# Kernel tuning notes

Hardware: AMD Instinct MI355X
Metric: run time of the kernel (lower is better)

Reference implementation:

```python
import jax, jax.numpy as jnp
import numpy as np

N_NODES = 100000
N_EDGES = 1600000
D_FEAT = 32
D_HID = 64
D_OUT = 64


def setup_inputs() -> dict:
    key = jax.random.key(0)
    ks = jax.random.split(key, 7)
    x = jax.random.normal(ks[0], (N_NODES, D_FEAT), dtype=jnp.float32)
    pos = jax.random.uniform(ks[1], (N_NODES, 3), dtype=jnp.float32) * 100.0
    # Fixed-size stand-in for radius_graph(pos, 5) output: (2, E) [source; target]
    edge_index = jax.random.randint(ks[2], (2, N_EDGES), 0, N_NODES, dtype=jnp.int64)
    d_in = D_FEAT + 3  # concat(x_j, pos_j - pos_i)
    W1 = jax.random.normal(ks[3], (d_in, D_HID), dtype=jnp.float32) / np.sqrt(d_in)
    b1 = jnp.zeros((D_HID,), dtype=jnp.float32)
    W2 = jax.random.normal(ks[4], (D_HID, D_OUT), dtype=jnp.float32) / np.sqrt(D_HID)
    b2 = jnp.zeros((D_OUT,), dtype=jnp.float32)
    return {"x": x, "pos": pos, "edge_index": edge_index,
            "W1": W1, "b1": b1, "W2": W2, "b2": b2}


def reference(x, pos, edge_index, W1, b1, W2, b2):
    n = x.shape[0]
    # PointNetConv default add_self_loops=True (radius_graph used loop=False)
    loops = jnp.arange(n, dtype=edge_index.dtype)
    src = jnp.concatenate([edge_index[0], loops])  # source j
    dst = jnp.concatenate([edge_index[1], loops])  # target i
    # gather: per-edge message input [E+N, d_feat+3]
    msg_in = jnp.concatenate([x[src], pos[src] - pos[dst]], axis=-1)
    # local_nn MLP
    h = jax.nn.relu(msg_in @ W1 + b1) @ W2 + b2
    # scatter: max-aggregate onto target nodes (PointConv aggr='max')
    out = jax.ops.segment_max(h, dst, num_segments=n)
    return out
```

## Files before the change

### kernel.cpp

```cpp
#include <hip/hip_runtime.h>
#include <math.h>

#define N_NODES 100000
#define N_EDGES 1600000
#define D_FEAT 32
#define D_HID 64
#define D_OUT 64
#define CAP 48
#define NPB 32
#define NBKT 3125
#define B1 256
#define E_PER_B1 6250
#define NB_NODE 1024

typedef _Float16 half8 __attribute__((ext_vector_type(8)));
typedef float f32x4  __attribute__((ext_vector_type(4)));

__device__ inline unsigned pk_subrelu(unsigned v, unsigned nq) {
    unsigned r;
    asm("v_pk_add_f16 %0, %1, %2\n\t"
        "v_pk_max_f16 %0, %0, 0"
        : "=v"(r) : "v"(v), "v"(nq));
    return r;
}

__global__ __launch_bounds__(256)
void node_kernel(const float* __restrict__ x,
                 const float* __restrict__ pos,
                 const float* __restrict__ W1,
                 const float* __restrict__ b1,
                 unsigned short* __restrict__ vb,
                 unsigned short* __restrict__ qb) {
    const int lane = threadIdx.x & 63;
    const int wid  = (blockIdx.x * blockDim.x + threadIdx.x) >> 6;
    const int nw   = (NB_NODE * 256) >> 6;

    float w[D_FEAT + 3];
#pragma unroll
    for (int f = 0; f < D_FEAT + 3; ++f)
        w[f] = W1[f * D_HID + lane];
    const float bb = b1[lane];

    for (int node = wid; node < N_NODES; node += nw) {
        const float* xr = x + (size_t)node * D_FEAT;
        float acc = bb;
#pragma unroll
        for (int f = 0; f < D_FEAT; ++f)
            acc = fmaf(xr[f], w[f], acc);

        const float* pr = pos + (size_t)node * 3;
        float qa = 0.0f;
#pragma unroll
        for (int p = 0; p < 3; ++p)
            qa = fmaf(pr[p], w[D_FEAT + p], qa);

        vb[(size_t)node * D_HID + lane] =
            __builtin_bit_cast(unsigned short, (_Float16)(acc + qa));
        qb[(size_t)node * D_HID + lane] =
            __builtin_bit_cast(unsigned short, (_Float16)(-qa));
    }
}

__global__ __launch_bounds__(1024)
void sort_kernel(const int* __restrict__ src,
                 const int* __restrict__ dst,
                 unsigned int* __restrict__ coarse,
                 int* __restrict__ dirT) {
    __shared__ int hist[NBKT];
    __shared__ int stage[E_PER_B1];
    __shared__ int wsum[16];

    const int tid  = threadIdx.x;
    const int lane = tid & 63;
    const int wv   = tid >> 6;
    const int e0   = blockIdx.x * E_PER_B1;

    for (int b = tid; b < NBKT; b += 1024) hist[b] = 0;
    __syncthreads();

    for (int e = e0 + tid; e < e0 + E_PER_B1; e += 1024)
        atomicAdd(&hist[dst[e] >> 5], 1);
    __syncthreads();

    const int i0 = tid * 4;
    int c[4];
    int sum = 0;
#pragma unroll
    for (int k = 0; k < 4; ++k) {
        c[k] = (i0 + k < NBKT) ? hist[i0 + k] : 0;
        sum += c[k];
    }
    int inc = sum;
#pragma unroll
    for (int d = 1; d < 64; d <<= 1) {
        int u = __shfl_up(inc, d, 64);
        if (lane >= d) inc += u;
    }
    if (lane == 63) wsum[wv] = inc;
    __syncthreads();
    if (wv == 0) {
        int s = (lane < 16) ? wsum[lane] : 0;
#pragma unroll
        for (int d = 1; d < 16; d <<= 1) {
            int u = __shfl_up(s, d, 64);
            if (lane >= d) s += u;
        }
        if (lane < 16) wsum[lane] = s;
    }
    __syncthreads();
    int excl = inc - sum + ((wv > 0) ? wsum[wv - 1] : 0);
#pragma unroll
    for (int k = 0; k < 4; ++k) {
        if (i0 + k < NBKT) hist[i0 + k] = excl;
        excl += c[k];
    }
    __syncthreads();

    for (int b = tid; b < NBKT; b += 1024)
        dirT[(size_t)b * B1 + blockIdx.x] = e0 + hist[b];
    __syncthreads();

    for (int e = e0 + tid; e < e0 + E_PER_B1; e += 1024) {
        int d = dst[e], s = src[e];
        int p = atomicAdd(&hist[d >> 5], 1);
        stage[p] = (int)(((unsigned)s << 5) | (unsigned)(d & 31));
    }
    __syncthreads();

    for (int i = tid; i < E_PER_B1; i += 1024)
        coarse[e0 + i] = (unsigned)stage[i];
}

__global__ __launch_bounds__(256)
void agg_kernel(const unsigned short* __restrict__ vb,
                const unsigned short* __restrict__ qb,
                const float* __restrict__ W2,
                const float* __restrict__ b2,
                const int* __restrict__ dirT,
                const unsigned int* __restrict__ coarse,
                float* __restrict__ out) {
    __shared__ int lcnt[NPB];
    __shared__ int lslots[NPB][CAP];

    const int tid  = threadIdx.x;
    const int lane = tid & 63;
    const int wave = tid >> 6;
    const int quad = lane >> 4;
    const int mrow = lane & 15;
    const int bkt  = blockIdx.x;
    const int nbase = bkt << 5;

    half8 bfrag[4][2];
#pragma unroll
    for (int t = 0; t < 4; ++t)
#pragma unroll
        for (int kh = 0; kh < 2; ++kh) {
            half8 f;
#pragma unroll
            for (int j = 0; j < 8; ++j)
                f[j] = (_Float16)W2[(kh * 32 + quad * 8 + j) * D_OUT + t * 16 + mrow];
            bfrag[t][kh] = f;
        }
    float bias[4];
#pragma unroll
    for (int t = 0; t < 4; ++t) bias[t] = b2[t * 16 + mrow];

    for (int i = tid; i < NPB; i += 256) lcnt[i] = 0;
    __syncthreads();
    {
        const int s0 = dirT[(size_t)bkt * B1 + tid];
        const int s1 = (bkt + 1 < NBKT) ? dirT[(size_t)(bkt + 1) * B1 + tid]
                                        : (tid + 1) * E_PER_B1;
        for (int j = s0; j < s1; ++j) {
            unsigned enc = coarse[j];
            int local = (int)(enc & 31u);
            int s     = (int)(enc >> 5);
            int p = atomicAdd(&lcnt[local], 1);
            if (p < CAP) lslots[local][p] = s;
        }
    }
    __syncthreads();

    for (int ln = wave; ln < NPB; ln += 4) {
        const int node = nbase + ln;

        const uint4 nq0 = *(const uint4*)(qb + (size_t)node * D_HID + quad * 8);
        const uint4 nq1 = *(const uint4*)(qb + (size_t)node * D_HID + 32 + quad * 8);

        int deg = lcnt[ln];
        if (deg > CAP) deg = CAP;
        const int rows = deg + 1;
        const int nbat = (rows + 15) >> 4;

        float rmax[4][4];
#pragma unroll
        for (int t = 0; t < 4; ++t)
#pragma unroll
            for (int r = 0; r < 4; ++r) rmax[t][r] = -INFINITY;

        for (int b = 0; b < nbat; ++b) {
            int idx = b * 16 + mrow;
            int idxc = (idx < CAP) ? idx : (CAP - 1);
            int s = (idx < deg) ? lslots[ln][idxc] : node;

            const uint4 v0 = *(const uint4*)(vb + (size_t)s * D_HID + quad * 8);
            const uint4 v1 = *(const uint4*)(vb + (size_t)s * D_HID + 32 + quad * 8);

            uint4 a0u, a1u;
            a0u.x = pk_subrelu(v0.x, nq0.x);
            a0u.y = pk_subrelu(v0.y, nq0.y);
            a0u.z = pk_subrelu(v0.z, nq0.z);
            a0u.w = pk_subrelu(v0.w, nq0.w);
            a1u.x = pk_subrelu(v1.x, nq1.x);
            a1u.y = pk_subrelu(v1.y, nq1.y);
            a1u.z = pk_subrelu(v1.z, nq1.z);
            a1u.w = pk_subrelu(v1.w, nq1.w);
            half8 a0 = __builtin_bit_cast(half8, a0u);
            half8 a1 = __builtin_bit_cast(half8, a1u);

#pragma unroll
            for (int t = 0; t < 4; ++t) {
                f32x4 acc = (f32x4){0.f, 0.f, 0.f, 0.f};
                acc = __builtin_amdgcn_mfma_f32_16x16x32_f16(a0, bfrag[t][0], acc, 0, 0, 0);
                acc = __builtin_amdgcn_mfma_f32_16x16x32_f16(a1, bfrag[t][1], acc, 0, 0, 0);
#pragma unroll
                for (int r = 0; r < 4; ++r)
                    rmax[t][r] = fmaxf(rmax[t][r], acc[r]);
            }
        }

        float fin[4];
#pragma unroll
        for (int t = 0; t < 4; ++t) {
            float m = fmaxf(fmaxf(rmax[t][0], rmax[t][1]), fmaxf(rmax[t][2], rmax[t][3]));
            m = fmaxf(m, __shfl_xor(m, 16, 64));
            m = fmaxf(m, __shfl_xor(m, 32, 64));
            fin[t] = m + bias[t];
        }
        float r = (quad == 0) ? fin[0] : (quad == 1) ? fin[1] : (quad == 2) ? fin[2] : fin[3];
        out[(size_t)node * D_OUT + lane] = r;
    }
}

extern "C" void kernel_launch(void* const* d_in, const int* in_sizes, int n_in,
                              void* d_out, int out_size, void* d_ws, size_t ws_size,
                              hipStream_t stream) {
    const float* x   = (const float*)d_in[0];
    const float* pos = (const float*)d_in[1];
    const int*   ei  = (const int*)d_in[2];
    const float* W1  = (const float*)d_in[3];
    const float* b1  = (const float*)d_in[4];
    const float* W2  = (const float*)d_in[5];
    const float* b2  = (const float*)d_in[6];
    float* out = (float*)d_out;

    char* ws = (char*)d_ws;
    unsigned short* vb   = (unsigned short*)ws;
    unsigned short* qb   = (unsigned short*)(ws + 12800000);
    unsigned int* coarse = (unsigned int*)(ws + 25600000);
    int*            dirT = (int*)(ws + 32000000);

    const int* src = ei;
    const int* dst = ei + N_EDGES;

    hipLaunchKernelGGL(sort_kernel, dim3(B1), dim3(1024), 0, stream,
                       src, dst, coarse, dirT);
    hipLaunchKernelGGL(node_kernel, dim3(NB_NODE), dim3(256), 0, stream,
                       x, pos, W1, b1, vb, qb);
    hipLaunchKernelGGL(agg_kernel, dim3(NBKT), dim3(256), 0, stream,
                       vb, qb, W2, b2, dirT, coarse, out);
}
```

Measured before the change: 199.6 us.

## Make aggregation kernel persistent with atomic work queue and pre-transposed fp16 W2

Turns the aggregation kernel into a persistent grid of 2048 blocks that claim 32-node buckets from a global atomic counter, so the per-block W2 fragment setup is paid once per block rather than once per bucket. W2 is also converted to fp16 and transposed once inside the sort kernel, so each block loads its MFMA B-fragments as vector loads instead of strided scalar float loads. This adds a memset, a global atomic and extra barriers per bucket, and with fewer resident blocks there may be less latency hiding for the gather loads.

```diff
diff --git a/kernel.cpp b/kernel.cpp
--- a/kernel.cpp
+++ b/kernel.cpp
@@ -12,6 +12,7 @@
 #define B1 256
 #define E_PER_B1 6250
 #define NB_NODE 1024
+#define AGG_B 2048
 
 typedef _Float16 half8 __attribute__((ext_vector_type(8)));
 typedef float f32x4  __attribute__((ext_vector_type(4)));
@@ -65,7 +66,9 @@
 void sort_kernel(const int* __restrict__ src,
                  const int* __restrict__ dst,
                  unsigned int* __restrict__ coarse,
-                 int* __restrict__ dirT) {
+                 int* __restrict__ dirT,
+                 const float* __restrict__ W2,
+                 unsigned short* __restrict__ W2T) {
     __shared__ int hist[NBKT];
     __shared__ int stage[E_PER_B1];
     __shared__ int wsum[16];
@@ -75,6 +78,14 @@
     const int wv   = tid >> 6;
     const int e0   = blockIdx.x * E_PER_B1;
 
+    if (blockIdx.x == 0) {
+        for (int i = tid; i < D_HID * D_OUT; i += 1024) {
+            float w = W2[i];
+            W2T[(size_t)(i & 63) * D_HID + (i >> 6)] =
+                __builtin_bit_cast(unsigned short, (_Float16)w);
+        }
+    }
+
     for (int b = tid; b < NBKT; b += 1024) hist[b] = 0;
     __syncthreads();
 
@@ -134,111 +145,117 @@
 __global__ __launch_bounds__(256)
 void agg_kernel(const unsigned short* __restrict__ vb,
                 const unsigned short* __restrict__ qb,
-                const float* __restrict__ W2,
+                const unsigned short* __restrict__ W2T,
                 const float* __restrict__ b2,
                 const int* __restrict__ dirT,
                 const unsigned int* __restrict__ coarse,
+                int* __restrict__ ctr,
                 float* __restrict__ out) {
     __shared__ int lcnt[NPB];
     __shared__ int lslots[NPB][CAP];
+    __shared__ int sbkt;
 
     const int tid  = threadIdx.x;
     const int lane = tid & 63;
     const int wave = tid >> 6;
     const int quad = lane >> 4;
     const int mrow = lane & 15;
-    const int bkt  = blockIdx.x;
-    const int nbase = bkt << 5;
 
     half8 bfrag[4][2];
 #pragma unroll
     for (int t = 0; t < 4; ++t)
 #pragma unroll
-        for (int kh = 0; kh < 2; ++kh) {
-            half8 f;
-#pragma unroll
-            for (int j = 0; j < 8; ++j)
-                f[j] = (_Float16)W2[(kh * 32 + quad * 8 + j) * D_OUT + t * 16 + mrow];
-            bfrag[t][kh] = f;
-        }
+        for (int kh = 0; kh < 2; ++kh)
+            bfrag[t][kh] = *(const half8*)(W2T + (size_t)(t * 16 + mrow) * D_HID
+                                               + kh * 32 + quad * 8);
     float bias[4];
 #pragma unroll
     for (int t = 0; t < 4; ++t) bias[t] = b2[t * 16 + mrow];
 
-    for (int i = tid; i < NPB; i += 256) lcnt[i] = 0;
-    __syncthreads();
-    {
-        const int s0 = dirT[(size_t)bkt * B1 + tid];
-        const int s1 = (bkt + 1 < NBKT) ? dirT[(size_t)(bkt + 1) * B1 + tid]
-                                        : (tid + 1) * E_PER_B1;
-        for (int j = s0; j < s1; ++j) {
-            unsigned enc = coarse[j];
-            int local = (int)(enc & 31u);
-            int s     = (int)(enc >> 5);
-            int p = atomicAdd(&lcnt[local], 1);
-            if (p < CAP) lslots[local][p] = s;
-        }
-    }
-    __syncthreads();
-
-    for (int ln = wave; ln < NPB; ln += 4) {
-        const int node = nbase + ln;
-
-        const uint4 nq0 = *(const uint4*)(qb + (size_t)node * D_HID + quad * 8);
-        const uint4 nq1 = *(const uint4*)(qb + (size_t)node * D_HID + 32 + quad * 8);
-
-        int deg = lcnt[ln];
-        if (deg > CAP) deg = CAP;
-        const int rows = deg + 1;
-        const int nbat = (rows + 15) >> 4;
-
-        float rmax[4][4];
-#pragma unroll
-        for (int t = 0; t < 4; ++t)
-#pragma unroll
-            for (int r = 0; r < 4; ++r) rmax[t][r] = -INFINITY;
-
-        for (int b = 0; b < nbat; ++b) {
-            int idx = b * 16 + mrow;
-            int idxc = (idx < CAP) ? idx : (CAP - 1);
-            int s = (idx < deg) ? lslots[ln][idxc] : node;
-
-            const uint4 v0 = *(const uint4*)(vb + (size_t)s * D_HID + quad * 8);
-            const uint4 v1 = *(const uint4*)(vb + (size_t)s * D_HID + 32 + quad * 8);
-
-            uint4 a0u, a1u;
-            a0u.x = pk_subrelu(v0.x, nq0.x);
-            a0u.y = pk_subrelu(v0.y, nq0.y);
-            a0u.z = pk_subrelu(v0.z, nq0.z);
-            a0u.w = pk_subrelu(v0.w, nq0.w);
-            a1u.x = pk_subrelu(v1.x, nq1.x);
-            a1u.y = pk_subrelu(v1.y, nq1.y);
-            a1u.z = pk_subrelu(v1.z, nq1.z);
-            a1u.w = pk_subrelu(v1.w, nq1.w);
-            half8 a0 = __builtin_bit_cast(half8, a0u);
-            half8 a1 = __builtin_bit_cast(half8, a1u);
-
+    while (true) {
+        if (tid == 0) sbkt = atomicAdd(ctr, 1);
+        __syncthreads();
+        const int bkt = sbkt;
+        if (bkt >= NBKT) break;
+        const int nbase = bkt << 5;
+
+        for (int i = tid; i < NPB; i += 256) lcnt[i] = 0;
+        __syncthreads();
+
+        {
+            const int s0 = dirT[(size_t)bkt * B1 + tid];
+            const int s1 = (bkt + 1 < NBKT) ? dirT[(size_t)(bkt + 1) * B1 + tid]
+                                            : (tid + 1) * E_PER_B1;
+            for (int j = s0; j < s1; ++j) {
+                unsigned enc = coarse[j];
+                int local = (int)(enc & 31u);
+                int s     = (int)(enc >> 5);
+                int p = atomicAdd(&lcnt[local], 1);
+                if (p < CAP) lslots[local][p] = s;
+            }
+        }
+        __syncthreads();
+
+        for (int ln = wave; ln < NPB; ln += 4) {
+            const int node = nbase + ln;
+
+            const uint4 nq0 = *(const uint4*)(qb + (size_t)node * D_HID + quad * 8);
+            const uint4 nq1 = *(const uint4*)(qb + (size_t)node * D_HID + 32 + quad * 8);
+
+            int deg = lcnt[ln];
+            if (deg > CAP) deg = CAP;
+            const int rows = deg + 1;
+            const int nbat = (rows + 15) >> 4;
+
+            float rmax[4][4];
+#pragma unroll
+            for (int t = 0; t < 4; ++t)
+#pragma unroll
+                for (int r = 0; r < 4; ++r) rmax[t][r] = -INFINITY;
+
+            for (int b = 0; b < nbat; ++b) {
+                int idx = b * 16 + mrow;
+                int idxc = (idx < CAP) ? idx : (CAP - 1);
+                int s = (idx < deg) ? lslots[ln][idxc] : node;
+
+                const uint4 v0 = *(const uint4*)(vb + (size_t)s * D_HID + quad * 8);
+                const uint4 v1 = *(const uint4*)(vb + (size_t)s * D_HID + 32 + quad * 8);
+
+                uint4 a0u, a1u;
+                a0u.x = pk_subrelu(v0.x, nq0.x);
+                a0u.y = pk_subrelu(v0.y, nq0.y);
+                a0u.z = pk_subrelu(v0.z, nq0.z);
+                a0u.w = pk_subrelu(v0.w, nq0.w);
+                a1u.x = pk_subrelu(v1.x, nq1.x);
+                a1u.y = pk_subrelu(v1.y, nq1.y);
+                a1u.z = pk_subrelu(v1.z, nq1.z);
+                a1u.w = pk_subrelu(v1.w, nq1.w);
+                half8 a0 = __builtin_bit_cast(half8, a0u);
+                half8 a1 = __builtin_bit_cast(half8, a1u);
+
+#pragma unroll
+                for (int t = 0; t < 4; ++t) {
+                    f32x4 acc = (f32x4){0.f, 0.f, 0.f, 0.f};
+                    acc = __builtin_amdgcn_mfma_f32_16x16x32_f16(a0, bfrag[t][0], acc, 0, 0, 0);
+                    acc = __builtin_amdgcn_mfma_f32_16x16x32_f16(a1, bfrag[t][1], acc, 0, 0, 0);
+#pragma unroll
+                    for (int r = 0; r < 4; ++r)
+                        rmax[t][r] = fmaxf(rmax[t][r], acc[r]);
+                }
+            }
+
+            float fin[4];
 #pragma unroll
             for (int t = 0; t < 4; ++t) {
-                f32x4 acc = (f32x4){0.f, 0.f, 0.f, 0.f};
-                acc = __builtin_amdgcn_mfma_f32_16x16x32_f16(a0, bfrag[t][0], acc, 0, 0, 0);
-                acc = __builtin_amdgcn_mfma_f32_16x16x32_f16(a1, bfrag[t][1], acc, 0, 0, 0);
-#pragma unroll
-                for (int r = 0; r < 4; ++r)
-                    rmax[t][r] = fmaxf(rmax[t][r], acc[r]);
+                float m = fmaxf(fmaxf(rmax[t][0], rmax[t][1]), fmaxf(rmax[t][2], rmax[t][3]));
+                m = fmaxf(m, __shfl_xor(m, 16, 64));
+                m = fmaxf(m, __shfl_xor(m, 32, 64));
+                fin[t] = m + bias[t];
             }
-        }
-
-        float fin[4];
-#pragma unroll
-        for (int t = 0; t < 4; ++t) {
-            float m = fmaxf(fmaxf(rmax[t][0], rmax[t][1]), fmaxf(rmax[t][2], rmax[t][3]));
-            m = fmaxf(m, __shfl_xor(m, 16, 64));
-            m = fmaxf(m, __shfl_xor(m, 32, 64));
-            fin[t] = m + bias[t];
-        }
-        float r = (quad == 0) ? fin[0] : (quad == 1) ? fin[1] : (quad == 2) ? fin[2] : fin[3];
-        out[(size_t)node * D_OUT + lane] = r;
+            float r = (quad == 0) ? fin[0] : (quad == 1) ? fin[1] : (quad == 2) ? fin[2] : fin[3];
+            out[(size_t)node * D_OUT + lane] = r;
+        }
+        __syncthreads();
     }
 }
 
@@ -259,14 +276,17 @@
     unsigned short* qb   = (unsigned short*)(ws + 12800000);
     unsigned int* coarse = (unsigned int*)(ws + 25600000);
     int*            dirT = (int*)(ws + 32000000);
+    unsigned short* W2T  = (unsigned short*)(ws + 35200000);
+    int*            ctr  = (int*)(ws + 35208192);
 
     const int* src = ei;
     const int* dst = ei + N_EDGES;
 
+    (void)hipMemsetAsync(ctr, 0, sizeof(int), stream);
     hipLaunchKernelGGL(sort_kernel, dim3(B1), dim3(1024), 0, stream,
-                       src, dst, coarse, dirT);
+                       src, dst, coarse, dirT, W2, W2T);
     hipLaunchKernelGGL(node_kernel, dim3(NB_NODE), dim3(256), 0, stream,
                        x, pos, W1, b1, vb, qb);
-    hipLaunchKernelGGL(agg_kernel, dim3(NBKT), dim3(256), 0, stream,
-                       vb, qb, W2, b2, dirT, coarse, out);
-}
+    hipLaunchKernelGGL(agg_kernel, dim3(AGG_B), dim3(256), 0, stream,
+                       vb, qb, W2T, b2, dirT, coarse, ctr, out);
+}
```

New measurement: 216.1 us. 1.08x slower.
